# Optimization experiments

Measured on AMD Instinct MI355X. Metric: run time of the kernel, lower is better.

## Reference

```python
import jax, jax.numpy as jnp
import numpy as np

ROUTING_ITER = 2
EPS = 1e-8


def squash(s, axis):
    # s * ||s||^2 / (1 + ||s||^2) / ||s||
    sq = jnp.sum(s * s, axis=axis, keepdims=True)
    return s * (sq / (1.0 + sq)) / jnp.sqrt(sq + EPS)


def setup_inputs() -> dict:
    key = jax.random.key(0)
    k1, k2 = jax.random.split(key)
    B, N_in, d_in = 64, 2048, 16
    J, D = 32, 16  # num_capsule, dim_capsule
    x = jax.random.normal(k1, (B, N_in, 1, d_in), dtype=jnp.float32)
    weight = jax.random.normal(k2, (1, N_in, J, D, d_in), dtype=jnp.float32) * 0.05
    return {"x": x, "weight": weight}


def reference(x, weight):
    # x: [B, N_in, 1, d_in]; weight: [1, N_in, J, D, d_in]
    # prediction vectors u[b,i,j,:] = W[i,j] @ x[b,i]
    u = jnp.einsum('ijde,bie->bijd', weight[0], x[:, :, 0, :])  # [B,N_in,J,D]
    B, N_in, J, D = u.shape

    # dynamic routing on stop_gradient(u)
    u_sg = jax.lax.stop_gradient(u)
    b = jnp.zeros((B, N_in, J, 1), dtype=u.dtype)
    for _ in range(ROUTING_ITER):
        c = jax.nn.softmax(b, axis=2)                      # [B,N_in,J,1]
        s = jnp.sum(u_sg * c, axis=1, keepdims=True)       # [B,1,J,D]
        v = squash(s, axis=2)                              # squash over capsule axis (faithful)
        b = b + jnp.sum(u_sg * v, axis=-1, keepdims=True)  # [B,N_in,J,1]

    c = jax.nn.softmax(b, axis=2)
    s = jnp.sum(u * c, axis=1)  # [B,J,D]
    return squash(s, axis=-1)
```

## Files before the change

kernel.cpp:

```cpp
#include <hip/hip_runtime.h>

typedef __attribute__((ext_vector_type(8))) short short8;
typedef __attribute__((ext_vector_type(4))) float f32x4;
typedef __attribute__((ext_vector_type(2))) float f32x2;
typedef __attribute__((ext_vector_type(4))) unsigned int uint4v;
typedef unsigned short u16;

#define NI 2048

__device__ __forceinline__ unsigned int packbf2(float a, float b){
  unsigned int ua = __float_as_uint(a), ub = __float_as_uint(b);
  unsigned int ra = (ua + 0x7FFFu + ((ua >> 16) & 1u)) >> 16;
  unsigned int rb = (ub + 0x7FFFu + ((ub >> 16) & 1u)) & 0xFFFF0000u;
  return ra | rb;
}
__device__ __forceinline__ float bflo(unsigned int p){ return __uint_as_float(p << 16); }
__device__ __forceinline__ float bfhi(unsigned int p){ return __uint_as_float(p & 0xFFFF0000u); }

__device__ __forceinline__ uint4v cvt8(const f32x4& a, const f32x4& b){
  uint4v p = { packbf2(a.x, a.y), packbf2(a.z, a.w),
               packbf2(b.x, b.y), packbf2(b.z, b.w) };
  return p;
}

__device__ __forceinline__ void gl_lds16(const void* g, void* l){
  __builtin_amdgcn_global_load_lds(
      (const __attribute__((address_space(1))) unsigned int*)g,
      (__attribute__((address_space(3))) unsigned int*)l, 16, 0, 0);
}

__global__ __launch_bounds__(256)
void caps_prep(const float* __restrict__ W, const float* __restrict__ X,
               u16* __restrict__ Wb, u16* __restrict__ Xb)
{
  const int bid = blockIdx.x;
  if (bid < 8192){
    size_t base = (size_t)bid * 2048 + (size_t)threadIdx.x * 8;
    f32x4 a = *(const f32x4*)(W + base);
    f32x4 b = *(const f32x4*)(W + base + 4);
    *(uint4v*)(Wb + base) = cvt8(a, b);
  } else {
    int p = (bid - 8192) * 256 + threadIdx.x;
    int i = p >> 6, b = p & 63;
    const float* src = X + ((size_t)b * NI + i) * 16;
    f32x4 a0 = *(const f32x4*)(src);
    f32x4 a1 = *(const f32x4*)(src + 4);
    f32x4 a2 = *(const f32x4*)(src + 8);
    f32x4 a3 = *(const f32x4*)(src + 12);
    *(uint4v*)(Xb + (size_t)p * 16)     = cvt8(a0, a1);
    *(uint4v*)(Xb + (size_t)p * 16 + 8) = cvt8(a2, a3);
  }
}

template<int MODE>
__global__ __launch_bounds__(256, 2)
void caps_pass_f(const u16* __restrict__ Wb,
                 const u16* __restrict__ Xb,
                 const float* __restrict__ vbuf,
                 float* __restrict__ partials, int CI)
{
  constexpr int WR = (MODE == 0) ? 2 : 1;
  __shared__ __align__(16) u16 sW[2][WR * 8192];
  __shared__ __align__(16) u16 sX[2][WR * 512];
  __shared__ float sSum[4][16];

  const int t     = threadIdx.x;
  const int w     = t >> 6;
  const int lane  = t & 63;
  const int wtile = w & 1;
  const int jhalf = w >> 1;
  const int lq    = lane >> 4;
  const int lb    = lane & 15;
  const int q1    = lq & 1;
  const int bhalf = blockIdx.x & 1;
  const int iblk  = blockIdx.x >> 1;
  const int bloc  = wtile * 16 + lb;
  const int bg    = bhalf * 32 + bloc;
  const size_t i0 = (size_t)iblk * (size_t)CI;

  const short8 zero8 = {0,0,0,0,0,0,0,0};
  const f32x4  zf4   = {0.f,0.f,0.f,0.f};

  f32x4 acc[16];
  #pragma unroll
  for (int tj = 0; tj < 16; ++tj) acc[tj] = zf4;

  unsigned int vpl[16], vph[16];
  if constexpr (MODE == 1){
    #pragma unroll
    for (int tj = 0; tj < 16; ++tj){
      f32x4 v = *(const f32x4*)(&vbuf[bg * 512 + (jhalf * 16 + tj) * 16 + lq * 4]);
      vpl[tj] = packbf2(v.x, v.y);
      vph[tj] = packbf2(v.z, v.w);
    }
  }

  auto stage = [&](int nb, size_t irow){
    #pragma unroll
    for (int rr = 0; rr < WR; ++rr){
      const u16* src = Wb + (irow + rr) * 8192 + (size_t)(w * 4) * 512;
      u16* dst = &sW[nb][rr * 8192 + w * 4 * 512];
      #pragma unroll
      for (int r = 0; r < 4; ++r)
        gl_lds16(src + r * 512 + lane * 8, dst + r * 512);
    }
    if (w >= 4 - WR){
      int rr = w - (4 - WR);
      gl_lds16(Xb + ((irow + rr) * 64 + (size_t)bhalf * 32) * 16 + lane * 8,
               &sX[nb][rr * 512]);
    }
  };

  const int NSTEP = CI / WR;
  stage(0, i0);
  __syncthreads();

  for (int s = 0; s < NSTEP; ++s){
    const int buf = s & 1;
    if (s + 1 < NSTEP) stage(buf ^ 1, i0 + (size_t)(s + 1) * WR);

    if constexpr (MODE == 0){
      const int rsel = lq >> 1;
      short8 bfrag = *(const short8*)(&sX[buf][rsel * 512 + bloc * 16 + q1 * 8]);
      #pragma unroll
      for (int tj = 0; tj < 16; ++tj){
        int j = jhalf * 16 + tj;
        short8 afrag = *(const short8*)(&sW[buf][rsel * 8192 + j * 256 + lb * 16 + q1 * 8]);
        acc[tj] = __builtin_amdgcn_mfma_f32_16x16x32_bf16(afrag, bfrag, acc[tj], 0, 0, 0);
      }
    } else {
      short8 bl8 = *(const short8*)(&sX[buf][bloc * 16 + q1 * 8]);
      short8 bfrag = (lq < 2) ? bl8 : zero8;
      f32x4 ut[16];
      float e[16];
      float ps = 0.f;
      #pragma unroll
      for (int tj = 0; tj < 16; ++tj){
        int j = jhalf * 16 + tj;
        short8 al8 = *(const short8*)(&sW[buf][j * 256 + lb * 16 + q1 * 8]);
        short8 afrag = (lq < 2) ? al8 : zero8;
        ut[tj] = __builtin_amdgcn_mfma_f32_16x16x32_bf16(afrag, bfrag, zf4, 0, 0, 0);
        float p = ut[tj].x * bflo(vpl[tj]) + ut[tj].y * bfhi(vpl[tj])
                + ut[tj].z * bflo(vph[tj]) + ut[tj].w * bfhi(vph[tj]);
        p += __shfl_xor(p, 16, 64);
        p += __shfl_xor(p, 32, 64);
        e[tj] = __expf(p);
        ps += e[tj];
      }
      if (lane < 16) sSum[w][lane] = ps;
      __syncthreads();
      float inv = 1.0f / (ps + sSum[w ^ 2][lb]);
      #pragma unroll
      for (int tj = 0; tj < 16; ++tj){
        float c = e[tj] * inv;
        acc[tj].x += c * ut[tj].x;
        acc[tj].y += c * ut[tj].y;
        acc[tj].z += c * ut[tj].z;
        acc[tj].w += c * ut[tj].w;
      }
    }
    __syncthreads();
  }

  float* dst = partials + ((size_t)blockIdx.x * 4 + (size_t)w) * 4096 + (size_t)lane * 64;
  #pragma unroll
  for (int tj = 0; tj < 16; ++tj) *(f32x4*)(dst + tj * 4) = acc[tj];
}

template<int MODE>
__global__ __launch_bounds__(256)
void caps_pass_legacy(const float* __restrict__ Wg, const float* __restrict__ Xg,
                      const float* __restrict__ vbuf, float* __restrict__ partials, int CI)
{
  __shared__ __align__(16) unsigned short sW[2][8192];
  __shared__ __align__(16) unsigned int   sXd[2][256];
  __shared__ float sLog[(MODE == 1) ? (32 * 33) : 4];
  const int t = threadIdx.x, w = t >> 6, lane = t & 63;
  const int wtile = w & 1, jhalf = w >> 1, lq = lane >> 4, lb = lane & 15, q1 = lq & 1;
  const int bhalf = blockIdx.x & 1, iblk = blockIdx.x >> 1;
  const int bloc = wtile * 16 + lb, bg = bhalf * 32 + bloc;
  const size_t i0 = (size_t)iblk * (size_t)CI;
  const short8 zero8 = {0,0,0,0,0,0,0,0};
  const f32x4 zf4 = {0.f,0.f,0.f,0.f};
  f32x4 acc[16];
  #pragma unroll
  for (int tj = 0; tj < 16; ++tj) acc[tj] = zf4;
  unsigned int vpl[16], vph[16];
  if constexpr (MODE == 1){
    #pragma unroll
    for (int tj = 0; tj < 16; ++tj){
      f32x4 v = *(const f32x4*)(&vbuf[bg * 512 + (jhalf * 16 + tj) * 16 + lq * 4]);
      vpl[tj] = packbf2(v.x, v.y); vph[tj] = packbf2(v.z, v.w);
    }
  }
  {
    const float* wsrc = Wg + i0 * 8192;
    #pragma unroll
    for (int r = 0; r < 4; ++r){
      int c = r * 256 + t;
      f32x4 a = *(const f32x4*)(&wsrc[c * 8]);
      f32x4 b = *(const f32x4*)(&wsrc[c * 8 + 4]);
      *(uint4v*)(&sW[0][c * 8]) = cvt8(a, b);
    }
    int bidx = bhalf * 32 + (t >> 3), e2 = t & 7;
    f32x2 xv = *(const f32x2*)(&Xg[((size_t)bidx * NI + i0) * 16 + e2 * 2]);
    sXd[0][t] = packbf2(xv.x, xv.y);
  }
  __syncthreads();
  for (int s = 0; s < CI; ++s){
    const int buf = s & 1;
    f32x4 wpa[4], wpb[4]; f32x2 xp;
    const bool more = (s + 1 < CI);
    if (more){
      const float* wsrc = Wg + (i0 + (size_t)(s + 1)) * 8192;
      #pragma unroll
      for (int r = 0; r < 4; ++r){
        int c = r * 256 + t;
        wpa[r] = *(const f32x4*)(&wsrc[c * 8]);
        wpb[r] = *(const f32x4*)(&wsrc[c * 8 + 4]);
      }
      int bidx = bhalf * 32 + (t >> 3), e2 = t & 7;
      xp = *(const f32x2*)(&Xg[((size_t)bidx * NI + i0 + s + 1) * 16 + e2 * 2]);
    }
    const unsigned short* xrow = (const unsigned short*)&sXd[buf][0];
    short8 bl8 = *(const short8*)(&xrow[bloc * 16 + q1 * 8]);
    short8 bfrag = (lq < 2) ? bl8 : zero8;
    if constexpr (MODE == 0){
      #pragma unroll
      for (int tj = 0; tj < 16; ++tj){
        int j = jhalf * 16 + tj;
        short8 al8 = *(const short8*)(&sW[buf][j * 256 + lb * 16 + q1 * 8]);
        short8 afrag = (lq < 2) ? al8 : zero8;
        acc[tj] = __builtin_amdgcn_mfma_f32_16x16x32_bf16(afrag, bfrag, acc[tj], 0, 0, 0);
      }
    } else {
      #pragma unroll
      for (int tj = 0; tj < 16; ++tj){
        int j = jhalf * 16 + tj;
        short8 al8 = *(const short8*)(&sW[buf][j * 256 + lb * 16 + q1 * 8]);
        short8 afrag = (lq < 2) ? al8 : zero8;
        f32x4 u = __builtin_amdgcn_mfma_f32_16x16x32_bf16(afrag, bfrag, zf4, 0, 0, 0);
        float p = u.x * bflo(vpl[tj]) + u.y * bfhi(vpl[tj])
                + u.z * bflo(vph[tj]) + u.w * bfhi(vph[tj]);
        p += __shfl_xor(p, 16, 64);
        p += __shfl_xor(p, 32, 64);
        if (lane < 16) sLog[bloc * 33 + j] = p;
      }
      __syncthreads();
      const float* logrow = &sLog[bloc * 33];
      float ssum = 0.f;
      #pragma unroll
      for (int jj = 0; jj < 32; ++jj) ssum += __expf(logrow[jj]);
      float inv = 1.0f / ssum;
      #pragma unroll
      for (int tj = 0; tj < 16; ++tj){
        int j = jhalf * 16 + tj;
        short8 al8 = *(const short8*)(&sW[buf][j * 256 + lb * 16 + q1 * 8]);
        short8 afrag = (lq < 2) ? al8 : zero8;
        f32x4 u = __builtin_amdgcn_mfma_f32_16x16x32_bf16(afrag, bfrag, zf4, 0, 0, 0);
        float c = __expf(logrow[j]) * inv;
        acc[tj].x += c * u.x; acc[tj].y += c * u.y;
        acc[tj].z += c * u.z; acc[tj].w += c * u.w;
      }
    }
    if (more){
      const int nb = buf ^ 1;
      #pragma unroll
      for (int r = 0; r < 4; ++r){
        int c = r * 256 + t;
        *(uint4v*)(&sW[nb][c * 8]) = cvt8(wpa[r], wpb[r]);
      }
      sXd[nb][t] = packbf2(xp.x, xp.y);
    }
    __syncthreads();
  }
  float* dst = partials + ((size_t)blockIdx.x * 4 + (size_t)w) * 4096 + (size_t)lane * 64;
  #pragma unroll
  for (int tj = 0; tj < 16; ++tj) *(f32x4*)(dst + tj * 4) = acc[tj];
}

template<int NBLK>
__global__ __launch_bounds__(128)
void caps_reduce(const float* __restrict__ partials, float* __restrict__ S_buf, float scale)
{
  const int T = blockIdx.x * 128 + threadIdx.x;
  float s0 = 0.f, s1 = 0.f, s2 = 0.f, s3 = 0.f;
  #pragma unroll
  for (int bl = 0; bl < NBLK; bl += 4){
    s0 += partials[(size_t)(bl + 0) * 32768 + T];
    s1 += partials[(size_t)(bl + 1) * 32768 + T];
    s2 += partials[(size_t)(bl + 2) * 32768 + T];
    s3 += partials[(size_t)(bl + 3) * 32768 + T];
  }
  float s = ((s0 + s1) + (s2 + s3)) * scale;
  const int bhalf = T >> 14, w = (T >> 12) & 3, l = (T >> 6) & 63, k = T & 63;
  const int b  = bhalf * 32 + (w & 1) * 16 + (l & 15);
  const int jd = ((w >> 1) * 16 + (k >> 2)) * 16 + ((l >> 4) << 2) + (k & 3);
  S_buf[b * 512 + jd] = s;
}

__global__ __launch_bounds__(256)
void caps_squash_j(const float* __restrict__ S, const float* __restrict__ vprev,
                   float* __restrict__ vout)
{
  const int b = blockIdx.x, t = threadIdx.x;
  __shared__ float sq[16];
  if (t < 16) sq[t] = 0.f;
  __syncthreads();
  float s0 = S[b * 512 + t], s1 = S[b * 512 + 256 + t];
  atomicAdd(&sq[t & 15], s0 * s0 + s1 * s1);
  __syncthreads();
  float q = sq[t & 15];
  float f = q / ((1.f + q) * sqrtf(q + 1e-8f));
  float v0 = s0 * f, v1 = s1 * f;
  if (vprev){ v0 += vprev[b * 512 + t]; v1 += vprev[b * 512 + 256 + t]; }
  vout[b * 512 + t] = v0;
  vout[b * 512 + 256 + t] = v1;
}

__global__ __launch_bounds__(256)
void caps_squash_d(const float* __restrict__ S, float* __restrict__ out)
{
  const int b = blockIdx.x, t = threadIdx.x;
  __shared__ float sq[32];
  if (t < 32) sq[t] = 0.f;
  __syncthreads();
  float s0 = S[b * 512 + t], s1 = S[b * 512 + 256 + t];
  atomicAdd(&sq[t >> 4], s0 * s0);
  atomicAdd(&sq[(t + 256) >> 4], s1 * s1);
  __syncthreads();
  float q0 = sq[t >> 4], q1 = sq[(t + 256) >> 4];
  out[b * 512 + t]       = s0 * q0 / ((1.f + q0) * sqrtf(q0 + 1e-8f));
  out[b * 512 + 256 + t] = s1 * q1 / ((1.f + q1) * sqrtf(q1 + 1e-8f));
}

extern "C" void kernel_launch(void* const* d_in, const int* in_sizes, int n_in,
                              void* d_out, int out_size, void* d_ws, size_t ws_size,
                              hipStream_t stream)
{
  const float* X = (const float*)d_in[0];
  const float* W = (const float*)d_in[1];
  float* wsf = (float*)d_ws;

  const size_t FP = (size_t)256 * 32768;
  const size_t WB_ELE = (size_t)NI * 8192, XB_ELE = (size_t)NI * 64 * 16;
  const size_t need_full = (FP + 3 * 32768) * 4 + (WB_ELE + XB_ELE) * 2;

  if (ws_size >= need_full){
    float* partials = wsf;
    float* sbuf = wsf + FP;
    float* v1   = sbuf + 32768;
    float* v12  = v1 + 32768;
    u16* Wb = (u16*)(v12 + 32768);
    u16* Xb = Wb + WB_ELE;

    caps_prep<<<dim3(8704), dim3(256), 0, stream>>>(W, X, Wb, Xb);

    caps_pass_f<0><<<dim3(512), dim3(256), 0, stream>>>(Wb, Xb, nullptr, partials, 8);
    caps_reduce<256><<<dim3(256), dim3(128), 0, stream>>>(partials, sbuf, 1.0f / 32.0f);
    caps_squash_j<<<dim3(64), dim3(256), 0, stream>>>(sbuf, nullptr, v1);

    caps_pass_f<1><<<dim3(512), dim3(256), 0, stream>>>(Wb, Xb, v1, partials, 8);
    caps_reduce<256><<<dim3(256), dim3(128), 0, stream>>>(partials, sbuf, 1.0f);
    caps_squash_j<<<dim3(64), dim3(256), 0, stream>>>(sbuf, v1, v12);

    caps_pass_f<1><<<dim3(512), dim3(256), 0, stream>>>(Wb, Xb, v12, partials, 8);
    caps_reduce<256><<<dim3(256), dim3(128), 0, stream>>>(partials, sbuf, 1.0f);
    caps_squash_d<<<dim3(64), dim3(256), 0, stream>>>(sbuf, (float*)d_out);
  } else {
    int NBI = 256;
    auto need = [](int nb){ return ((size_t)nb * 32768 + 3 * 32768) * 4; };
    if (ws_size < need(256)){
      if      (ws_size >= need(64)) NBI = 64;
      else if (ws_size >= need(16)) NBI = 16;
      else                          NBI = 4;
    }
    const int CI = NI / NBI;
    float* partials = wsf;
    float* sbuf = wsf + (size_t)NBI * 32768;
    float* v1   = sbuf + 32768;
    float* v12  = v1 + 32768;
    auto reduce = [&](float scale){
      if      (NBI == 256) caps_reduce<256><<<dim3(256), dim3(128), 0, stream>>>(partials, sbuf, scale);
      else if (NBI ==  64) caps_reduce< 64><<<dim3(256), dim3(128), 0, stream>>>(partials, sbuf, scale);
      else if (NBI ==  16) caps_reduce< 16><<<dim3(256), dim3(128), 0, stream>>>(partials, sbuf, scale);
      else                 caps_reduce<  4><<<dim3(256), dim3(128), 0, stream>>>(partials, sbuf, scale);
    };
    caps_pass_legacy<0><<<dim3(2 * NBI), dim3(256), 0, stream>>>(W, X, nullptr, partials, CI);
    reduce(1.0f / 32.0f);
    caps_squash_j<<<dim3(64), dim3(256), 0, stream>>>(sbuf, nullptr, v1);
    caps_pass_legacy<1><<<dim3(2 * NBI), dim3(256), 0, stream>>>(W, X, v1, partials, CI);
    reduce(1.0f);
    caps_squash_j<<<dim3(64), dim3(256), 0, stream>>>(sbuf, v1, v12);
    caps_pass_legacy<1><<<dim3(2 * NBI), dim3(256), 0, stream>>>(W, X, v12, partials, CI);
    reduce(1.0f);
    caps_squash_d<<<dim3(64), dim3(256), 0, stream>>>(sbuf, (float*)d_out);
  }
}
```

Measured before the change: 232.4 us.

## Fuse capsule routing into one persistent kernel with grid-wide barriers

```diff
diff --git a/kernel.cpp b/kernel.cpp
--- a/kernel.cpp
+++ b/kernel.cpp
@@ -28,6 +28,228 @@
       (const __attribute__((address_space(1))) unsigned int*)g,
       (__attribute__((address_space(3))) unsigned int*)l, 16, 0, 0);
 }
+
+
+#define FUSED_SMEM 150656
+
+template<int MODE>
+__device__ __forceinline__ void pass_phase(
+    const u16* __restrict__ sW, const u16* __restrict__ sX,
+    float* __restrict__ sSumA, float* __restrict__ sSumB,
+    const float* __restrict__ Sv1, const float* __restrict__ qv1,
+    const float* __restrict__ Sv2, const float* __restrict__ qv2,
+    float* __restrict__ partials, int blk, int t)
+{
+  const int w = t >> 6, lane = t & 63;
+  const int wtile = w & 1, jhalf = (w >> 1) & 1, bh = w >> 2;
+  const int lq = lane >> 4, lb = lane & 15, qs = lq & 1;
+  const int bg = bh * 32 + wtile * 16 + lb;
+  const short8 zero8 = {0,0,0,0,0,0,0,0};
+  const f32x4 zf4 = {0.f,0.f,0.f,0.f};
+
+  f32x4 acc[16];
+  #pragma unroll
+  for (int tj = 0; tj < 16; ++tj) acc[tj] = zf4;
+
+  unsigned int vpl[16], vph[16];
+  if constexpr (MODE >= 1){
+    f32x4 qa = *(const f32x4*)(qv1 + bg * 16 + lq * 4);
+    f32x4 fa;
+    fa.x = qa.x / ((1.f + qa.x) * sqrtf(qa.x + 1e-8f));
+    fa.y = qa.y / ((1.f + qa.y) * sqrtf(qa.y + 1e-8f));
+    fa.z = qa.z / ((1.f + qa.z) * sqrtf(qa.z + 1e-8f));
+    fa.w = qa.w / ((1.f + qa.w) * sqrtf(qa.w + 1e-8f));
+    f32x4 fb = zf4;
+    if constexpr (MODE == 2){
+      f32x4 qb = *(const f32x4*)(qv2 + bg * 16 + lq * 4);
+      fb.x = qb.x / ((1.f + qb.x) * sqrtf(qb.x + 1e-8f));
+      fb.y = qb.y / ((1.f + qb.y) * sqrtf(qb.y + 1e-8f));
+      fb.z = qb.z / ((1.f + qb.z) * sqrtf(qb.z + 1e-8f));
+      fb.w = qb.w / ((1.f + qb.w) * sqrtf(qb.w + 1e-8f));
+    }
+    #pragma unroll
+    for (int tj = 0; tj < 16; ++tj){
+      int jd = (jhalf * 16 + tj) * 16 + lq * 4;
+      f32x4 sv = *(const f32x4*)(Sv1 + bg * 512 + jd);
+      f32x4 v;
+      v.x = sv.x * fa.x; v.y = sv.y * fa.y; v.z = sv.z * fa.z; v.w = sv.w * fa.w;
+      if constexpr (MODE == 2){
+        f32x4 s2 = *(const f32x4*)(Sv2 + bg * 512 + jd);
+        v.x += s2.x * fb.x; v.y += s2.y * fb.y; v.z += s2.z * fb.z; v.w += s2.w * fb.w;
+      }
+      vpl[tj] = packbf2(v.x, v.y);
+      vph[tj] = packbf2(v.z, v.w);
+    }
+  }
+
+  if constexpr (MODE == 0){
+    const int rsel = lq >> 1;
+    #pragma unroll
+    for (int s = 0; s < 4; ++s){
+      const u16* wrow = sW + (size_t)(2 * s + rsel) * 8192;
+      const u16* xrow = sX + (size_t)(2 * s + rsel) * 1024;
+      short8 bfrag = *(const short8*)(xrow + bg * 16 + qs * 8);
+      #pragma unroll
+      for (int tj = 0; tj < 16; ++tj){
+        int j = jhalf * 16 + tj;
+        short8 afrag = *(const short8*)(wrow + j * 256 + lb * 16 + qs * 8);
+        acc[tj] = __builtin_amdgcn_mfma_f32_16x16x32_bf16(afrag, bfrag, acc[tj], 0, 0, 0);
+      }
+    }
+  } else {
+    for (int s = 0; s < 8; ++s){
+      const u16* wrow = sW + (size_t)s * 8192;
+      const u16* xrow = sX + (size_t)s * 1024;
+      short8 bl8 = *(const short8*)(xrow + bg * 16 + qs * 8);
+      short8 bfrag = (lq < 2) ? bl8 : zero8;
+      f32x4 ut[16];
+      float e[16];
+      float ps = 0.f;
+      #pragma unroll
+      for (int tj = 0; tj < 16; ++tj){
+        int j = jhalf * 16 + tj;
+        short8 afrag = *(const short8*)(wrow + j * 256 + lb * 16 + qs * 8);
+        ut[tj] = __builtin_amdgcn_mfma_f32_16x16x32_bf16(afrag, bfrag, zf4, 0, 0, 0);
+        float p = ut[tj].x * bflo(vpl[tj]) + ut[tj].y * bfhi(vpl[tj])
+                + ut[tj].z * bflo(vph[tj]) + ut[tj].w * bfhi(vph[tj]);
+        p += __shfl_xor(p, 16, 64);
+        p += __shfl_xor(p, 32, 64);
+        e[tj] = __expf(p);
+        ps += e[tj];
+      }
+      float* sS = (s & 1) ? sSumB : sSumA;
+      if (lane < 16) sS[w * 16 + lane] = ps;
+      __syncthreads();
+      float inv = 1.0f / (ps + sS[(w ^ 2) * 16 + lb]);
+      #pragma unroll
+      for (int tj = 0; tj < 16; ++tj){
+        float c = e[tj] * inv;
+        acc[tj].x += c * ut[tj].x;
+        acc[tj].y += c * ut[tj].y;
+        acc[tj].z += c * ut[tj].z;
+        acc[tj].w += c * ut[tj].w;
+      }
+    }
+  }
+
+  float* dst = partials + ((size_t)blk * 8 + (size_t)w) * 4096 + (size_t)lane * 64;
+  #pragma unroll
+  for (int tj = 0; tj < 16; ++tj) *(f32x4*)(dst + tj * 4) = acc[tj];
+}
+
+__device__ __forceinline__ void reduce_phase(
+    const float* __restrict__ partials, float* __restrict__ S,
+    float* __restrict__ qbuf, float scale, float* __restrict__ sRed,
+    int blk, int t)
+{
+  const int o = blk * 128 + (t & 127);
+  const int quarter = t >> 7;
+  const float* src = partials + (size_t)quarter * 64 * 32768 + (size_t)o;
+  float s = 0.f;
+  #pragma unroll 16
+  for (int p = 0; p < 64; ++p) s += src[(size_t)p * 32768];
+  sRed[t] = s;
+  __syncthreads();
+  if (t < 128){
+    float tot = ((sRed[t] + sRed[t + 128]) + (sRed[t + 256] + sRed[t + 384])) * scale;
+    const int bh = o >> 14, wd = (o >> 12) & 3, ln = (o >> 6) & 63, k = o & 63;
+    const int b = bh * 32 + (wd & 1) * 16 + (ln & 15);
+    const int j = (wd >> 1) * 16 + (k >> 2);
+    const int d = ((ln >> 4) << 2) + (k & 3);
+    S[b * 512 + j * 16 + d] = tot;
+    if (qbuf) atomicAdd(qbuf + b * 16 + d, tot * tot);
+  }
+  __syncthreads();
+}
+
+__global__ __launch_bounds__(512, 2)
+void caps_fused(const float* __restrict__ X, const float* __restrict__ W,
+                unsigned int* __restrict__ gcnt,
+                float* __restrict__ qb1, float* __restrict__ qb2,
+                float* __restrict__ S1, float* __restrict__ S2, float* __restrict__ S3,
+                float* __restrict__ partials, float* __restrict__ out)
+{
+  extern __shared__ __align__(16) char smem[];
+  u16* sW = (u16*)smem;
+  u16* sX = (u16*)(smem + 131072);
+  float* sSumA = (float*)(smem + 147456);
+  float* sSumB = sSumA + 128;
+  float* sRed  = sSumB + 128;
+  float* sq    = sRed + 512;
+
+  const int t = threadIdx.x;
+  const int blk = blockIdx.x;
+  const size_t i0 = (size_t)blk * 8;
+
+  {
+    const float* wsrc = W + i0 * 8192;
+    #pragma unroll
+    for (int k = 0; k < 16; ++k){
+      int idx = k * 4096 + t * 8;
+      f32x4 a = *(const f32x4*)(wsrc + idx);
+      f32x4 b = *(const f32x4*)(wsrc + idx + 4);
+      *(uint4v*)(sW + idx) = cvt8(a, b);
+    }
+    int r = t >> 6, b = t & 63;
+    const float* xs = X + ((size_t)b * NI + i0 + (size_t)r) * 16;
+    f32x4 a0 = *(const f32x4*)(xs);
+    f32x4 a1 = *(const f32x4*)(xs + 4);
+    f32x4 a2 = *(const f32x4*)(xs + 8);
+    f32x4 a3 = *(const f32x4*)(xs + 12);
+    *(uint4v*)(sX + t * 16)     = cvt8(a0, a1);
+    *(uint4v*)(sX + t * 16 + 8) = cvt8(a2, a3);
+  }
+  __syncthreads();
+
+  unsigned int gen = 0;
+  auto gridsync = [&](){
+    ++gen;
+    __syncthreads();
+    if (t == 0){
+      __threadfence();
+      __hip_atomic_fetch_add(gcnt, 1u, __ATOMIC_ACQ_REL, __HIP_MEMORY_SCOPE_AGENT);
+      const unsigned int target = gen * 256u;
+      while (__hip_atomic_load(gcnt, __ATOMIC_ACQUIRE, __HIP_MEMORY_SCOPE_AGENT) < target)
+        __builtin_amdgcn_s_sleep(2);
+      __threadfence();
+    }
+    __syncthreads();
+  };
+
+  pass_phase<0>(sW, sX, sSumA, sSumB, nullptr, nullptr, nullptr, nullptr, partials, blk, t);
+  gridsync();
+  reduce_phase(partials, S1, qb1, 1.0f / 32.0f, sRed, blk, t);
+  gridsync();
+
+  pass_phase<1>(sW, sX, sSumA, sSumB, S1, qb1, nullptr, nullptr, partials, blk, t);
+  gridsync();
+  reduce_phase(partials, S2, qb2, 1.0f, sRed, blk, t);
+  gridsync();
+
+  pass_phase<2>(sW, sX, sSumA, sSumB, S1, qb1, S2, qb2, partials, blk, t);
+  gridsync();
+  reduce_phase(partials, S3, nullptr, 1.0f, sRed, blk, t);
+  gridsync();
+
+  if (blk < 64){
+    if (t < 32) sq[t] = 0.f;
+    __syncthreads();
+    float s0 = 0.f, s1 = 0.f;
+    if (t < 256){
+      s0 = S3[blk * 512 + t];
+      s1 = S3[blk * 512 + 256 + t];
+      atomicAdd(&sq[t >> 4], s0 * s0);
+      atomicAdd(&sq[(t + 256) >> 4], s1 * s1);
+    }
+    __syncthreads();
+    if (t < 256){
+      float a = sq[t >> 4], c = sq[(t + 256) >> 4];
+      out[blk * 512 + t]       = s0 * (a / ((1.f + a) * sqrtf(a + 1e-8f)));
+      out[blk * 512 + 256 + t] = s1 * (c / ((1.f + c) * sqrtf(c + 1e-8f)));
+    }
+  }
+}
+
 
 __global__ __launch_bounds__(256)
 void caps_prep(const float* __restrict__ W, const float* __restrict__ X,
@@ -341,6 +563,35 @@
   const float* X = (const float*)d_in[0];
   const float* W = (const float*)d_in[1];
   float* wsf = (float*)d_ws;
+
+  const size_t OF_Q1   = 64;
+  const size_t OF_Q2   = OF_Q1 + 1024;
+  const size_t OF_S1   = OF_Q2 + 1024;
+  const size_t OF_S2   = OF_S1 + 32768;
+  const size_t OF_S3   = OF_S2 + 32768;
+  const size_t OF_PART = OF_S3 + 32768;
+  const size_t FUSED_FLOATS = OF_PART + (size_t)256 * 32768;
+
+  static int fused_ok = -1;
+  if (fused_ok < 0){
+    fused_ok = 0;
+    hipFuncSetAttribute(reinterpret_cast<const void*>(caps_fused),
+                        hipFuncAttributeMaxDynamicSharedMemorySize, FUSED_SMEM);
+    int dev = 0, ncu = 0, nb = 0;
+    hipGetDevice(&dev);
+    hipDeviceGetAttribute(&ncu, hipDeviceAttributeMultiprocessorCount, dev);
+    hipError_t e = hipOccupancyMaxActiveBlocksPerMultiprocessor(
+        &nb, caps_fused, 512, (size_t)FUSED_SMEM);
+    if (e == hipSuccess && nb >= 1 && ncu >= 256) fused_ok = 1;
+  }
+
+  if (fused_ok == 1 && ws_size >= FUSED_FLOATS * 4){
+    hipMemsetAsync(d_ws, 0, (64 + 1024 + 1024) * 4, stream);
+    caps_fused<<<dim3(256), dim3(512), FUSED_SMEM, stream>>>(
+        X, W, (unsigned int*)wsf, wsf + OF_Q1, wsf + OF_Q2,
+        wsf + OF_S1, wsf + OF_S2, wsf + OF_S3, wsf + OF_PART, (float*)d_out);
+    return;
+  }
 
   const size_t FP = (size_t)256 * 32768;
   const size_t WB_ELE = (size_t)NI * 8192, XB_ELE = (size_t)NI * 64 * 16;
```

After: 232.1 us. No clear change (-0.1%).
